# Kernel optimization log

Hardware: AMD Instinct MI355X
Metric: run time of the kernel (lower is better)

The kernel has to match this reference:

```python
import jax, jax.numpy as jnp
import numpy as np

D_MODEL = 1024
N_HEADS = 16
THETA = 10000.0


def _rope(x, token_positions):
    # x: (b, h, s, d_k); token_positions: (b, s)
    d_k = x.shape[-1]
    powers = jnp.arange(0, d_k, 2, dtype=jnp.float32) / d_k        # (d_k/2,)
    freqs = 1.0 / (THETA ** powers)
    ang = token_positions.astype(jnp.float32)[..., None] * freqs   # (b, s, d_k/2)
    cos = jnp.cos(ang)[:, None, :, :].astype(x.dtype)              # (b, 1, s, d_k/2)
    sin = jnp.sin(ang)[:, None, :, :].astype(x.dtype)
    x_even = x[..., ::2]
    x_odd = x[..., 1::2]
    r1 = x_even * cos - x_odd * sin
    r2 = x_even * sin + x_odd * cos
    # interleave back to (..., d_k)
    return jnp.stack([r1, r2], axis=-1).reshape(x.shape)


def reference(x, token_positions, wq, wk, wv, wo):
    B, S, D = x.shape
    H = N_HEADS
    d_k = D // H

    def proj(w):
        y = jnp.einsum('bsi,oi->bso', x, w)
        return y.reshape(B, S, H, d_k).transpose(0, 2, 1, 3)  # (b, h, s, d_k)

    q = _rope(proj(wq), token_positions)
    k = _rope(proj(wk), token_positions)
    v = proj(wv)

    scale = 1.0 / jnp.sqrt(jnp.asarray(d_k, dtype=x.dtype))
    score = jnp.einsum('bhqd,bhkd->bhqk', q, k) * scale  # (b, h, s, s)
    causal = jnp.tril(jnp.ones((S, S), dtype=bool))
    score = jnp.where(causal, score, -jnp.inf)
    probs = jax.nn.softmax(score, axis=-1)
    attn = jnp.einsum('bhqk,bhkd->bhqd', probs, v)
    attn = attn.transpose(0, 2, 1, 3).reshape(B, S, D)
    return jnp.einsum('bsi,oi->bso', attn, wo)


def setup_inputs() -> dict:
    key = jax.random.key(0)
    ks = jax.random.split(key, 6)
    B, S, D = 2, 2048, D_MODEL
    std = (2.0 / (D + D)) ** 0.5
    x = jax.random.normal(ks[0], (B, S, D), dtype=jnp.float32)
    token_positions = jnp.broadcast_to(jnp.arange(S, dtype=jnp.int32), (B, S))
    wq = jax.random.normal(ks[1], (D, D), dtype=jnp.float32) * std
    wk = jax.random.normal(ks[2], (D, D), dtype=jnp.float32) * std
    wv = jax.random.normal(ks[3], (D, D), dtype=jnp.float32) * std
    wo = jax.random.normal(ks[4], (D, D), dtype=jnp.float32) * std
    return {"x": x, "token_positions": token_positions, "wq": wq, "wk": wk, "wv": wv, "wo": wo}
```

## Files before the change

kernel.cpp:

```cpp
#include <hip/hip_runtime.h>
#include <hip/hip_bf16.h>

typedef unsigned short u16;
typedef unsigned int u32;
typedef short short8 __attribute__((ext_vector_type(8)));
typedef u16 u16x8 __attribute__((ext_vector_type(8)));
typedef u16 u16x4 __attribute__((ext_vector_type(4)));
typedef u32 u32x4 __attribute__((ext_vector_type(4)));
typedef float f32x4 __attribute__((ext_vector_type(4)));
typedef float f32x16 __attribute__((ext_vector_type(16)));

#define MFMA(a, b, c) __builtin_amdgcn_mfma_f32_16x16x32_bf16((a), (b), (c), 0, 0, 0)
#define MFMA32(a, b, c) __builtin_amdgcn_mfma_f32_32x32x16_bf16((a), (b), (c), 0, 0, 0)

#define QSCALE 0.18033688011112042f

__device__ __forceinline__ u16 f2bf(float f) {
  unsigned u = __float_as_uint(f);
  unsigned r = (u + 0x7fffu + ((u >> 16) & 1u)) >> 16;
  return (u16)r;
}
__device__ __forceinline__ float bf2f(u16 h) {
  return __uint_as_float(((unsigned)h) << 16);
}
__device__ __forceinline__ float exp2hw(float x) {
  float r;
  asm("v_exp_f32 %0, %1" : "=v"(r) : "v"(x));
  return r;
}
__device__ __forceinline__ u32 cvtpk(float lo, float hi) {
  u32 d;
  asm("v_cvt_pk_bf16_f32 %0, %1, %2" : "=v"(d) : "v"(lo), "v"(hi));
  return d;
}
__device__ __forceinline__ void plswap(u32& a, u32& b) {
  asm volatile("v_permlane32_swap_b32 %0, %1" : "+v"(a), "+v"(b));
}
__device__ __forceinline__ void async16(const void* g, void* l) {
  __builtin_amdgcn_global_load_lds(
      (const __attribute__((address_space(1))) void*)g,
      (__attribute__((address_space(3))) void*)l, 16, 0, 0);
}
__device__ __forceinline__ f32x16 zero16() {
  f32x16 z;
#pragma unroll
  for (int i = 0; i < 16; i++) z[i] = 0.f;
  return z;
}
#define WAITV(N) asm volatile("s_waitcnt vmcnt(" #N ")" ::: "memory")
#define WAITL0() asm volatile("s_waitcnt lgkmcnt(0)" ::: "memory")
#define BAR() __builtin_amdgcn_s_barrier()
#define PRIO1 __builtin_amdgcn_s_setprio(1)
#define PRIO0 __builtin_amdgcn_s_setprio(0)

__global__ __launch_bounds__(256) void convert_kernel(
    const float* __restrict__ x, const float* __restrict__ wq,
    const float* __restrict__ wk, const float* __restrict__ wv,
    const float* __restrict__ wo, u16* __restrict__ ws) {
  int blk = blockIdx.x;
  const float* src; u16* dst;
  if (blk < 2048)      { src = x;  dst = ws; }
  else if (blk < 2560) { src = wq; dst = ws + 4194304;               blk -= 2048; }
  else if (blk < 3072) { src = wk; dst = ws + 4194304 + 1048576;     blk -= 2560; }
  else if (blk < 3584) { src = wv; dst = ws + 4194304 + 2 * 1048576; blk -= 3072; }
  else                 { src = wo; dst = ws + 4194304 + 3 * 1048576; blk -= 3584; }
  int idx = (blk * 256 + threadIdx.x) * 8;
  float4 v0 = *(const float4*)(src + idx);
  float4 v1 = *(const float4*)(src + idx + 4);
  u16x8 o;
  o[0] = f2bf(v0.x); o[1] = f2bf(v0.y); o[2] = f2bf(v0.z); o[3] = f2bf(v0.w);
  o[4] = f2bf(v1.x); o[5] = f2bf(v1.y); o[6] = f2bf(v1.z); o[7] = f2bf(v1.w);
  *(u16x8*)(dst + idx) = o;
}

__global__ __launch_bounds__(256) void rope_table(const int* __restrict__ tp,
                                                  float* __restrict__ tab) {
  int t = blockIdx.x * 256 + threadIdx.x;
  int bs = t >> 5, p = t & 31;
  float freq = exp2hw(-(float)p * 0.4152410118609203f);
  float ang = (float)tp[bs] * freq;
  float sn, cs;
  sincosf(ang, &sn, &cs);
  tab[bs * 64 + p * 2] = cs;
  tab[bs * 64 + p * 2 + 1] = sn;
}

__global__ __launch_bounds__(512, 2) void gemm_qkv256(
    const u16* __restrict__ xb, const u16* __restrict__ wqb,
    const u16* __restrict__ wkb, const u16* __restrict__ wvb,
    const float* __restrict__ tab, u16* __restrict__ qb, u16* __restrict__ kb,
    u16* __restrict__ vt) {
  __shared__ u16 As[2][2][8192];
  __shared__ u16 Bs[2][2][8192];
  const int tid = threadIdx.x, lane = tid & 63, wid = tid >> 6;
  const int wm = wid >> 2, wn = wid & 3;
  const int g = lane >> 4, r = lane & 15;
  const int z = blockIdx.z;
  const u16* Ag = xb;
  const u16* Bg = (z == 0) ? wqb : (z == 1) ? wkb : wvb;
  const int rowBase = blockIdx.y << 8, colBase = blockIdx.x << 8;

  const int c0 = tid, c1 = tid + 512;
  const int sr0 = c0 >> 3, sk0 = ((c0 & 7) ^ (sr0 & 7)) * 8;
  const int sr1 = c1 >> 3, sk1 = ((c1 & 7) ^ (sr1 & 7)) * 8;

#define STG_A(BUF, H, T)                                                      \
  do {                                                                        \
    async16(Ag + (size_t)(rowBase + (H)*128 + sr0) * 1024 + (T)*64 + sk0,     \
            (char*)As[BUF][H] + c0 * 16);                                     \
    async16(Ag + (size_t)(rowBase + (H)*128 + sr1) * 1024 + (T)*64 + sk1,     \
            (char*)As[BUF][H] + c1 * 16);                                     \
  } while (0)
#define STG_B(BUF, H, T)                                                      \
  do {                                                                        \
    async16(Bg + (size_t)(colBase + (H)*128 + sr0) * 1024 + (T)*64 + sk0,     \
            (char*)Bs[BUF][H] + c0 * 16);                                     \
    async16(Bg + (size_t)(colBase + (H)*128 + sr1) * 1024 + (T)*64 + sk1,     \
            (char*)Bs[BUF][H] + c1 * 16);                                     \
  } while (0)

  f32x4 acc[8][4];
#pragma unroll
  for (int m = 0; m < 8; m++)
#pragma unroll
    for (int n = 0; n < 4; n++) acc[m][n] = (f32x4){0.f, 0.f, 0.f, 0.f};
  short8 af[4][2], bfr[4][2];

#define RD_A(CUR, MH)                                                         \
  do {                                                                        \
    _Pragma("unroll") for (int mi = 0; mi < 4; mi++) {                        \
      int ra = (MH)*64 + mi * 16 + r;                                         \
      const u16* p = As[CUR][wm] + ra * 64;                                   \
      int sw = (ra & 7) << 3;                                                 \
      af[mi][0] = *(const short8*)(p + ((g << 3) ^ sw));                      \
      af[mi][1] = *(const short8*)(p + (((4 + g) << 3) ^ sw));                \
    }                                                                         \
  } while (0)
#define RD_B(CUR, NP)                                                         \
  do {                                                                        \
    _Pragma("unroll") for (int ni = 0; ni < 2; ni++) {                        \
      int cb = wn * 64 + ((NP)*2 + ni) * 16 + r;                              \
      const u16* p = Bs[CUR][cb >> 7] + (cb & 127) * 64;                      \
      int sw = (cb & 7) << 3;                                                 \
      bfr[(NP)*2 + ni][0] = *(const short8*)(p + ((g << 3) ^ sw));            \
      bfr[(NP)*2 + ni][1] = *(const short8*)(p + (((4 + g) << 3) ^ sw));      \
    }                                                                         \
  } while (0)
#define MM16(MH, NP)                                                          \
  do {                                                                        \
    _Pragma("unroll") for (int mi = 0; mi < 4; mi++)                          \
        _Pragma("unroll") for (int ni = 0; ni < 2; ni++) {                    \
      acc[(MH)*4 + mi][(NP)*2 + ni] = MFMA(af[mi][0], bfr[(NP)*2 + ni][0],    \
                                           acc[(MH)*4 + mi][(NP)*2 + ni]);    \
      acc[(MH)*4 + mi][(NP)*2 + ni] = MFMA(af[mi][1], bfr[(NP)*2 + ni][1],    \
                                           acc[(MH)*4 + mi][(NP)*2 + ni]);    \
    }                                                                         \
  } while (0)

  STG_A(0, 0, 0); STG_A(0, 1, 0); STG_B(0, 0, 0); STG_B(0, 1, 0);
  STG_A(1, 0, 1); STG_A(1, 1, 1);
  WAITV(4);
  BAR();

  for (int t = 0; t < 16; ++t) {
    const int cur = t & 1, nxt = cur ^ 1;
    RD_A(cur, 0);
    RD_B(cur, 0); RD_B(cur, 1);
    if (t < 15) { STG_B(nxt, 0, t + 1); STG_B(nxt, 1, t + 1); }
    BAR(); WAITL0();
    PRIO1; MM16(0, 0); MM16(0, 1); PRIO0; BAR();
    RD_A(cur, 1);
    if (t < 14) {
      STG_A(cur, 0, t + 2); STG_A(cur, 1, t + 2);
      WAITV(4);
    } else {
      WAITV(0);
    }
    BAR(); WAITL0();
    PRIO1; MM16(1, 0); MM16(1, 1); PRIO0; BAR();
  }
#undef STG_A
#undef STG_B
#undef RD_A
#undef RD_B
#undef MM16

  if (z < 2) {
    u16* dst = z ? kb : qb;
    const float qs = z ? 1.0f : QSCALE;
#pragma unroll
    for (int m = 0; m < 8; m++)
#pragma unroll
      for (int n = 0; n < 4; n++) {
        const int col = colBase + wn * 64 + n * 16 + r;
        const int p2 = (col >> 1) & 31;
        const bool odd = col & 1;
#pragma unroll
        for (int i = 0; i < 4; i++) {
          const int row = rowBase + wm * 128 + m * 16 + g * 4 + i;
          float2 cssn = *(const float2*)(tab + row * 64 + p2 * 2);
          float v = acc[m][n][i];
          float part = __shfl_xor(v, 1);
          float res = odd ? (part * cssn.y + v * cssn.x)
                          : (v * cssn.x - part * cssn.y);
          dst[(size_t)row * 1024 + col] = f2bf(res * qs);
        }
      }
  } else {
#pragma unroll
    for (int m = 0; m < 8; m++)
#pragma unroll
      for (int n = 0; n < 4; n++)
#pragma unroll
        for (int i = 0; i < 4; i++) {
          int row = rowBase + wm * 128 + m * 16 + g * 4 + i;
          int col = colBase + wn * 64 + n * 16 + r;
          int b = row >> 11, s = row & 2047;
          vt[(size_t)((b * 16 + (col >> 6)) * 64 + (col & 63)) * 2048 + s] =
              f2bf(acc[m][n][i]);
        }
  }
}

__device__ __forceinline__ void gemm_tile(const u16* __restrict__ A,
                                          const u16* __restrict__ Bm, int K,
                                          int rowBase, int colBase, u16* As,
                                          u16* Bs, f32x4 acc[4][4]) {
  const int tid = threadIdx.x;
  const int lane = tid & 63, wid = tid >> 6;
  const int wr = wid >> 1, wc = wid & 1;
  const int g = lane >> 4, r = lane & 15;

#pragma unroll
  for (int m = 0; m < 4; m++)
#pragma unroll
    for (int n = 0; n < 4; n++) acc[m][n] = (f32x4){0.f, 0.f, 0.f, 0.f};

#define GSTAGE(KT, BUF)                                                       \
  do {                                                                        \
    _Pragma("unroll") for (int i_ = 0; i_ < 4; ++i_) {                        \
      int c = i_ * 256 + tid;                                                 \
      int row = c >> 3, kc = (c & 7) ^ (row & 7);                             \
      async16(A + (size_t)(rowBase + row) * K + ((KT) << 6) + kc * 8,         \
              (char*)As + (BUF)*16384 + c * 16);                              \
    }                                                                         \
    _Pragma("unroll") for (int i_ = 0; i_ < 4; ++i_) {                        \
      int c = i_ * 256 + tid;                                                 \
      int row = c >> 3, kc = (c & 7) ^ (row & 7);                             \
      async16(Bm + (size_t)(colBase + row) * K + ((KT) << 6) + kc * 8,        \
              (char*)Bs + (BUF)*16384 + c * 16);                              \
    }                                                                         \
  } while (0)

  const int nkt = K >> 6;
  GSTAGE(0, 0);
  for (int kt = 0; kt < nkt; ++kt) {
    const int cur = kt & 1;
    if (kt + 1 < nkt) {
      GSTAGE(kt + 1, cur ^ 1);
      WAITV(8);
    } else {
      WAITV(0);
    }
    BAR();
    const u16* Ab = As + cur * 8192;
    const u16* Bb = Bs + cur * 8192;
#pragma unroll
    for (int ks = 0; ks < 2; ++ks) {
      short8 af[4], bfr[4];
#pragma unroll
      for (int m = 0; m < 4; m++) {
        int rr = wr * 64 + m * 16 + r;
        af[m] = *(const short8*)(Ab + rr * 64 + (((ks * 4 + g) ^ (rr & 7)) << 3));
      }
#pragma unroll
      for (int n = 0; n < 4; n++) {
        int rr = wc * 64 + n * 16 + r;
        bfr[n] = *(const short8*)(Bb + rr * 64 + (((ks * 4 + g) ^ (rr & 7)) << 3));
      }
#pragma unroll
      for (int m = 0; m < 4; m++)
#pragma unroll
        for (int n = 0; n < 4; n++)
          acc[m][n] = MFMA(af[m], bfr[n], acc[m][n]);
    }
    WAITL0();
    BAR();
  }
#undef GSTAGE
}

__global__ __launch_bounds__(256, 2) void attn_kernel(
    const u16* __restrict__ qg, const u16* __restrict__ kg,
    const u16* __restrict__ vt, u16* __restrict__ ab) {
  __shared__ u16 Ks[2][64 * 64];
  __shared__ u16 Vs[2][64 * 64];
  const int tid = threadIdx.x, wid = tid >> 6, lane = tid & 63;
  const int q5 = lane & 31, hi = lane >> 5;
  const int ak = blockIdx.x >> 5, bh = blockIdx.x & 31;
  const int a = ak >> 1, k = ak & 1;
  const int b = bh >> 4, h = bh & 15;
  const int base = (wid < 2) ? a : (15 - a);
  const int rb = base * 128 + k * 64 + (wid & 1) * 32;
  const int cmax = rb >> 5;
  const int jend = 30 - 2 * a + k;
  const int qrow = (b << 11) + rb + q5;

  short8 bq[4];
  {
    const u16* qp = qg + (size_t)qrow * 1024 + (h << 6) + hi * 8;
    bq[0] = *(const short8*)(qp);
    bq[1] = *(const short8*)(qp + 16);
    bq[2] = *(const short8*)(qp + 32);
    bq[3] = *(const short8*)(qp + 48);
  }
  f32x16 accO0 = zero16(), accO1 = zero16();
  float m_r = -1e30f, l_r = 0.f;

#define STAGE(JT, BUF)                                                        \
  do {                                                                        \
    _Pragma("unroll") for (int i_ = 0; i_ < 2; i_++) {                        \
      int c = i_ * 256 + tid;                                                 \
      int row = c >> 3, cc = (c & 7) ^ (row & 7);                             \
      async16(kg + (size_t)((b << 11) + ((JT) << 6) + row) * 1024 +           \
                  (h << 6) + cc * 8,                                          \
              (char*)Ks[BUF] + c * 16);                                       \
      async16(vt + (size_t)((bh << 6) + row) * 2048 + ((JT) << 6) + cc * 8,   \
              (char*)Vs[BUF] + c * 16);                                       \
    }                                                                         \
  } while (0)

  STAGE(0, 0);

  for (int j = 0; j <= jend; ++j) {
    const int cur = j & 1;
    if (j < jend) {
      STAGE(j + 1, cur ^ 1);
      WAITV(4);
    } else {
      WAITV(0);
    }
    BAR();
    if (2 * j <= cmax) {
      const u16* Kb = Ks[cur];
      const u16* Vb = Vs[cur];
      const bool has1 = (2 * j + 1 <= cmax);
      const int rsw = (q5 & 7) << 3;
      f32x16 s0 = zero16(), s1 = zero16();
      PRIO1;
#pragma unroll
      for (int kk = 0; kk < 4; kk++) {
        short8 kf =
            *(const short8*)(Kb + q5 * 64 + ((((kk << 1) + hi) << 3) ^ rsw));
        s0 = MFMA32(kf, bq[kk], s0);
      }
      PRIO0;
      if (has1) {
        PRIO1;
#pragma unroll
        for (int kk = 0; kk < 4; kk++) {
          short8 kf = *(const short8*)(Kb + (32 + q5) * 64 +
                                       ((((kk << 1) + hi) << 3) ^ rsw));
          s1 = MFMA32(kf, bq[kk], s1);
        }
        PRIO0;
      }
      if (2 * j == cmax) {
#pragma unroll
        for (int rg = 0; rg < 16; rg++) {
          int rowk = (rg & 3) + 8 * (rg >> 2) + 4 * hi;
          if (rowk > q5) s0[rg] = -1e30f;
        }
      } else if (2 * j + 1 == cmax) {
#pragma unroll
        for (int rg = 0; rg < 16; rg++) {
          int rowk = (rg & 3) + 8 * (rg >> 2) + 4 * hi;
          if (rowk > q5) s1[rg] = -1e30f;
        }
      }
      float pmax = s0[0];
#pragma unroll
      for (int rg = 1; rg < 16; rg++) pmax = fmaxf(pmax, s0[rg]);
      if (has1) {
#pragma unroll
        for (int rg = 0; rg < 16; rg++) pmax = fmaxf(pmax, s1[rg]);
      }
      pmax = fmaxf(pmax, __shfl_xor(pmax, 32));
      if (!__all(pmax <= m_r + 8.0f)) {
        float mn = fmaxf(m_r, pmax);
        float sc = exp2hw(m_r - mn);
        l_r *= sc;
#pragma unroll
        for (int rg = 0; rg < 16; rg++) {
          accO0[rg] *= sc;
          accO1[rg] *= sc;
        }
        m_r = mn;
      }
      float rs = 0.f;
      u32 pw00[4], pw01[4], pw10[4], pw11[4];
#define PACK(SREG, OUT, S16)                                                  \
  do {                                                                        \
    float p0 = exp2hw(SREG[(S16)*8 + 0] - m_r);                               \
    float p1 = exp2hw(SREG[(S16)*8 + 1] - m_r);                               \
    float p2 = exp2hw(SREG[(S16)*8 + 2] - m_r);                               \
    float p3 = exp2hw(SREG[(S16)*8 + 3] - m_r);                               \
    float p4 = exp2hw(SREG[(S16)*8 + 4] - m_r);                               \
    float p5 = exp2hw(SREG[(S16)*8 + 5] - m_r);                               \
    float p6 = exp2hw(SREG[(S16)*8 + 6] - m_r);                               \
    float p7 = exp2hw(SREG[(S16)*8 + 7] - m_r);                               \
    rs += ((p0 + p1) + (p2 + p3)) + ((p4 + p5) + (p6 + p7));                  \
    u32 X = cvtpk(p0, p1), Y = cvtpk(p2, p3);                                 \
    u32 U = cvtpk(p4, p5), W = cvtpk(p6, p7);                                 \
    plswap(X, U);                                                             \
    plswap(Y, W);                                                             \
    OUT[0] = X; OUT[1] = Y; OUT[2] = U; OUT[3] = W;                           \
  } while (0)
      PACK(s0, pw00, 0);
      PACK(s0, pw01, 1);
      if (has1) {
        PACK(s1, pw10, 0);
        PACK(s1, pw11, 1);
      }
#undef PACK
      rs += __shfl_xor(rs, 32);
      l_r += rs;
#define PVSTEP(PW, CH)                                                        \
  do {                                                                        \
    u32x4 pv_ = {PW[0], PW[1], PW[2], PW[3]};                                 \
    short8 pb_ = __builtin_bit_cast(short8, pv_);                             \
    short8 v0_ =                                                              \
        *(const short8*)(Vb + q5 * 64 + ((((CH) + hi) << 3) ^ rsw));          \
    short8 v1_ = *(const short8*)(Vb + (32 + q5) * 64 +                       \
                                  ((((CH) + hi) << 3) ^ rsw));                \
    accO0 = MFMA32(v0_, pb_, accO0);                                          \
    accO1 = MFMA32(v1_, pb_, accO1);                                          \
  } while (0)
      PRIO1;
      PVSTEP(pw00, 0);
      PVSTEP(pw01, 2);
      if (has1) {
        PVSTEP(pw10, 4);
        PVSTEP(pw11, 6);
      }
      PRIO0;
#undef PVSTEP
    }
    WAITL0();
    BAR();
  }
#undef STAGE

  float inv = 1.0f / l_r;
#pragma unroll
  for (int qd = 0; qd < 4; qd++) {
    u16x4 o0, o1;
#pragma unroll
    for (int e = 0; e < 4; e++) {
      o0[e] = f2bf(accO0[qd * 4 + e] * inv);
      o1[e] = f2bf(accO1[qd * 4 + e] * inv);
    }
    u16* op = ab + (size_t)qrow * 1024 + (h << 6) + qd * 8 + hi * 4;
    *(u16x4*)(op) = o0;
    *(u16x4*)(op + 32) = o1;
  }
}

__global__ __launch_bounds__(256) void gemm_ao(const u16* __restrict__ ab,
                                               const u16* __restrict__ wob,
                                               float* __restrict__ out) {
  __shared__ u16 As[2][128 * 64], Bs[2][128 * 64];
  f32x4 acc[4][4];
  gemm_tile(ab, wob, 1024, blockIdx.y * 128, blockIdx.x * 128, As[0], Bs[0], acc);
  const int lane = threadIdx.x & 63, wid = threadIdx.x >> 6;
  const int wr = wid >> 1, wc = wid & 1, g = lane >> 4, r = lane & 15;
  const int rowB = blockIdx.y * 128 + wr * 64;
  const int colB = blockIdx.x * 128 + wc * 64;
#pragma unroll
  for (int m = 0; m < 4; m++)
#pragma unroll
    for (int n = 0; n < 4; n++)
#pragma unroll
      for (int i = 0; i < 4; i++)
        out[(size_t)(rowB + m * 16 + g * 4 + i) * 1024 + colB + n * 16 + r] =
            acc[m][n][i];
}

extern "C" void kernel_launch(void* const* d_in, const int* in_sizes, int n_in,
                              void* d_out, int out_size, void* d_ws,
                              size_t ws_size, hipStream_t stream) {
  const float* x = (const float*)d_in[0];
  const int* tp = (const int*)d_in[1];
  const float* wq = (const float*)d_in[2];
  const float* wk = (const float*)d_in[3];
  const float* wv = (const float*)d_in[4];
  const float* wo = (const float*)d_in[5];
  float* out = (float*)d_out;

  u16* ws = (u16*)d_ws;
  u16* xb = ws;
  u16* wqb = xb + 4194304;
  u16* wkb = wqb + 1048576;
  u16* wvb = wkb + 1048576;
  u16* wob = wvb + 1048576;
  u16* qb = wob + 1048576;
  u16* kb = qb + 4194304;
  u16* vtb = kb + 4194304;
  u16* ab = vtb + 4194304;
  float* tab = (float*)ab;

  convert_kernel<<<4096, 256, 0, stream>>>(x, wq, wk, wv, wo, ws);
  rope_table<<<512, 256, 0, stream>>>(tp, tab);
  gemm_qkv256<<<dim3(4, 16, 3), 512, 0, stream>>>(xb, wqb, wkb, wvb, tab, qb,
                                                  kb, vtb);
  attn_kernel<<<512, 256, 0, stream>>>(qb, kb, vtb, ab);
  gemm_ao<<<dim3(8, 32), 256, 0, stream>>>(ab, wob, out);
}
```

Before: 124.1 us.

## Split attention KV range across two blocks and merge partials (split-K flash)

Each attention work item is split into two blocks that process alternating KV tiles, which doubles the grid from 512 to 1024 blocks to fill the GPU better. Occupancy hint is raised to 4 blocks per CU. Unnormalized bf16 partial outputs plus per-row max and sum are written to scratch buffers that reuse the xb/wqb/wkb workspace. A new merge kernel combines the two partials with log-sum-exp weights. This adds an extra kernel launch, extra global traffic, and bf16 rounding of the unnormalized partials.

```diff
diff --git a/kernel.cpp b/kernel.cpp
--- a/kernel.cpp
+++ b/kernel.cpp
@@ -290,15 +290,16 @@
 #undef GSTAGE
 }
 
-__global__ __launch_bounds__(256, 2) void attn_kernel(
+__global__ __launch_bounds__(256, 4) void attn_kernel(
     const u16* __restrict__ qg, const u16* __restrict__ kg,
-    const u16* __restrict__ vt, u16* __restrict__ ab) {
+    const u16* __restrict__ vt, u16* __restrict__ p0, u16* __restrict__ p1,
+    float* __restrict__ mbuf, float* __restrict__ lbuf) {
   __shared__ u16 Ks[2][64 * 64];
   __shared__ u16 Vs[2][64 * 64];
   const int tid = threadIdx.x, wid = tid >> 6, lane = tid & 63;
   const int q5 = lane & 31, hi = lane >> 5;
-  const int ak = blockIdx.x >> 5, bh = blockIdx.x & 31;
-  const int a = ak >> 1, k = ak & 1;
+  const int akc = blockIdx.x >> 5, bh = blockIdx.x & 31;
+  const int a = akc >> 2, k = (akc >> 1) & 1, c = akc & 1;
   const int b = bh >> 4, h = bh & 15;
   const int base = (wid < 2) ? a : (15 - a);
   const int rb = base * 128 + k * 64 + (wid & 1) * 32;
@@ -320,31 +321,31 @@
 #define STAGE(JT, BUF)                                                        \
   do {                                                                        \
     _Pragma("unroll") for (int i_ = 0; i_ < 2; i_++) {                        \
-      int c = i_ * 256 + tid;                                                 \
-      int row = c >> 3, cc = (c & 7) ^ (row & 7);                             \
+      int cc_ = i_ * 256 + tid;                                               \
+      int row = cc_ >> 3, cc = (cc_ & 7) ^ (row & 7);                         \
       async16(kg + (size_t)((b << 11) + ((JT) << 6) + row) * 1024 +           \
                   (h << 6) + cc * 8,                                          \
-              (char*)Ks[BUF] + c * 16);                                       \
+              (char*)Ks[BUF] + cc_ * 16);                                     \
       async16(vt + (size_t)((bh << 6) + row) * 2048 + ((JT) << 6) + cc * 8,   \
-              (char*)Vs[BUF] + c * 16);                                       \
+              (char*)Vs[BUF] + cc_ * 16);                                     \
     }                                                                         \
   } while (0)
 
-  STAGE(0, 0);
-
-  for (int j = 0; j <= jend; ++j) {
-    const int cur = j & 1;
-    if (j < jend) {
-      STAGE(j + 1, cur ^ 1);
+  if (c <= jend) STAGE(c, 0);
+
+  for (int jj = c; jj <= jend; jj += 2) {
+    const int cur = ((jj - c) >> 1) & 1;
+    if (jj + 2 <= jend) {
+      STAGE(jj + 2, cur ^ 1);
       WAITV(4);
     } else {
       WAITV(0);
     }
     BAR();
-    if (2 * j <= cmax) {
+    if (2 * jj <= cmax) {
       const u16* Kb = Ks[cur];
       const u16* Vb = Vs[cur];
-      const bool has1 = (2 * j + 1 <= cmax);
+      const bool has1 = (2 * jj + 1 <= cmax);
       const int rsw = (q5 & 7) << 3;
       f32x16 s0 = zero16(), s1 = zero16();
       PRIO1;
@@ -365,13 +366,13 @@
         }
         PRIO0;
       }
-      if (2 * j == cmax) {
+      if (2 * jj == cmax) {
 #pragma unroll
         for (int rg = 0; rg < 16; rg++) {
           int rowk = (rg & 3) + 8 * (rg >> 2) + 4 * hi;
           if (rowk > q5) s0[rg] = -1e30f;
         }
-      } else if (2 * j + 1 == cmax) {
+      } else if (2 * jj + 1 == cmax) {
 #pragma unroll
         for (int rg = 0; rg < 16; rg++) {
           int rowk = (rg & 3) + 8 * (rg >> 2) + 4 * hi;
@@ -401,17 +402,17 @@
       u32 pw00[4], pw01[4], pw10[4], pw11[4];
 #define PACK(SREG, OUT, S16)                                                  \
   do {                                                                        \
-    float p0 = exp2hw(SREG[(S16)*8 + 0] - m_r);                               \
-    float p1 = exp2hw(SREG[(S16)*8 + 1] - m_r);                               \
-    float p2 = exp2hw(SREG[(S16)*8 + 2] - m_r);                               \
-    float p3 = exp2hw(SREG[(S16)*8 + 3] - m_r);                               \
-    float p4 = exp2hw(SREG[(S16)*8 + 4] - m_r);                               \
-    float p5 = exp2hw(SREG[(S16)*8 + 5] - m_r);                               \
-    float p6 = exp2hw(SREG[(S16)*8 + 6] - m_r);                               \
-    float p7 = exp2hw(SREG[(S16)*8 + 7] - m_r);                               \
-    rs += ((p0 + p1) + (p2 + p3)) + ((p4 + p5) + (p6 + p7));                  \
-    u32 X = cvtpk(p0, p1), Y = cvtpk(p2, p3);                                 \
-    u32 U = cvtpk(p4, p5), W = cvtpk(p6, p7);                                 \
+    float pp0 = exp2hw(SREG[(S16)*8 + 0] - m_r);                              \
+    float pp1 = exp2hw(SREG[(S16)*8 + 1] - m_r);                              \
+    float pp2 = exp2hw(SREG[(S16)*8 + 2] - m_r);                              \
+    float pp3 = exp2hw(SREG[(S16)*8 + 3] - m_r);                              \
+    float pp4 = exp2hw(SREG[(S16)*8 + 4] - m_r);                              \
+    float pp5 = exp2hw(SREG[(S16)*8 + 5] - m_r);                              \
+    float pp6 = exp2hw(SREG[(S16)*8 + 6] - m_r);                              \
+    float pp7 = exp2hw(SREG[(S16)*8 + 7] - m_r);                              \
+    rs += ((pp0 + pp1) + (pp2 + pp3)) + ((pp4 + pp5) + (pp6 + pp7));          \
+    u32 X = cvtpk(pp0, pp1), Y = cvtpk(pp2, pp3);                             \
+    u32 U = cvtpk(pp4, pp5), W = cvtpk(pp6, pp7);                             \
     plswap(X, U);                                                             \
     plswap(Y, W);                                                             \
     OUT[0] = X; OUT[1] = Y; OUT[2] = U; OUT[3] = W;                           \
@@ -451,19 +452,47 @@
   }
 #undef STAGE
 
-  float inv = 1.0f / l_r;
+  u16* pout = c ? p1 : p0;
 #pragma unroll
   for (int qd = 0; qd < 4; qd++) {
     u16x4 o0, o1;
 #pragma unroll
     for (int e = 0; e < 4; e++) {
-      o0[e] = f2bf(accO0[qd * 4 + e] * inv);
-      o1[e] = f2bf(accO1[qd * 4 + e] * inv);
+      o0[e] = f2bf(accO0[qd * 4 + e]);
+      o1[e] = f2bf(accO1[qd * 4 + e]);
     }
-    u16* op = ab + (size_t)qrow * 1024 + (h << 6) + qd * 8 + hi * 4;
+    u16* op = pout + (size_t)qrow * 1024 + (h << 6) + qd * 8 + hi * 4;
     *(u16x4*)(op) = o0;
     *(u16x4*)(op + 32) = o1;
   }
+  if (hi == 0) {
+    int mli = c * 65536 + (bh << 11) + rb + q5;
+    mbuf[mli] = m_r;
+    lbuf[mli] = l_r;
+  }
+}
+
+__global__ __launch_bounds__(256) void attn_merge(const u16* __restrict__ p1,
+                                                  const float* __restrict__ mbuf,
+                                                  const float* __restrict__ lbuf,
+                                                  u16* __restrict__ ab) {
+  int t = blockIdx.x * 256 + threadIdx.x;
+  int dg = t & 7, row = t >> 3;
+  int bh = row >> 11, s = row & 2047;
+  int b = bh >> 4, h = bh & 15;
+  size_t addr = (size_t)((b << 11) + s) * 1024 + (h << 6) + dg * 8;
+  float m0 = mbuf[row], m1 = mbuf[65536 + row];
+  float l0 = lbuf[row], l1 = lbuf[65536 + row];
+  float m = fmaxf(m0, m1);
+  float w0 = exp2hw(m0 - m), w1 = exp2hw(m1 - m);
+  float inv = 1.0f / (l0 * w0 + l1 * w1);
+  u16x8 o0 = *(const u16x8*)(ab + addr);
+  u16x8 o1 = *(const u16x8*)(p1 + addr);
+  u16x8 o;
+#pragma unroll
+  for (int i = 0; i < 8; i++)
+    o[i] = f2bf((bf2f(o0[i]) * w0 + bf2f(o1[i]) * w1) * inv);
+  *(u16x8*)(ab + addr) = o;
 }
 
 __global__ __launch_bounds__(256) void gemm_ao(const u16* __restrict__ ab,
@@ -508,11 +537,14 @@
   u16* vtb = kb + 4194304;
   u16* ab = vtb + 4194304;
   float* tab = (float*)ab;
+  float* mbuf = (float*)wqb;
+  float* lbuf = (float*)wkb;
 
   convert_kernel<<<4096, 256, 0, stream>>>(x, wq, wk, wv, wo, ws);
   rope_table<<<512, 256, 0, stream>>>(tp, tab);
   gemm_qkv256<<<dim3(4, 16, 3), 512, 0, stream>>>(xb, wqb, wkb, wvb, tab, qb,
                                                   kb, vtb);
-  attn_kernel<<<512, 256, 0, stream>>>(qb, kb, vtb, ab);
+  attn_kernel<<<1024, 256, 0, stream>>>(qb, kb, vtb, ab, xb, mbuf, lbuf);
+  attn_merge<<<2048, 256, 0, stream>>>(xb, mbuf, lbuf, ab);
   gemm_ao<<<dim3(8, 32), 256, 0, stream>>>(ab, wob, out);
 }
```

New measurement: 118.0 us. -4.9%, faster.
